# Performance work log

Hardware: AMD Instinct MI355X
Metric: run time of the kernel (lower is better)

The kernel has to match this reference:

```python
import jax, jax.numpy as jnp
import numpy as np

B, T, C = 8, 2048, 512

def setup_inputs() -> dict:
    key = jax.random.key(0)
    ks = jax.random.split(key, 16)
    def n(k, shape, s=0.02):
        return jax.random.normal(k, shape, dtype=jnp.float32) * s
    inp = {
        'x_l': jax.random.normal(ks[0], (B, T, C), jnp.float32),
        'x_r': jax.random.normal(ks[1], (B, T, C), jnp.float32),
    }
    i = 2
    for name in ['lp1', 'rp1', 'lp2', 'rp2']:
        inp[name + '_w1'] = n(ks[i], (C, C))       # pointwise conv1d weight (out,in)
        inp[name + '_b1'] = jnp.zeros((C,), jnp.float32)
        inp[name + '_w2'] = n(ks[i + 1], (C, 3))   # depthwise conv k=3 weight per channel
        inp[name + '_b2'] = jnp.zeros((C,), jnp.float32)
        i += 2
    inp['lp3_w'] = n(ks[i], (C, C)); inp['lp3_b'] = jnp.zeros((C,), jnp.float32)
    inp['rp3_w'] = n(ks[i + 1], (C, C)); inp['rp3_b'] = jnp.zeros((C,), jnp.float32)
    return inp

def _proj(x, w1, b1, w2, b2):
    # x: (B,T,C). Pointwise conv1d (1x1) then depthwise conv1d k=3, pad=1 over T.
    h = jnp.einsum('btc,dc->btd', x, w1) + b1
    hp = jnp.pad(h, ((0, 0), (1, 1), (0, 0)))
    # cross-correlation: tap 0 -> t-1, tap 1 -> t, tap 2 -> t+1 (matches torch Conv1d)
    return hp[:, :-2, :] * w2[:, 0] + hp[:, 1:-1, :] * w2[:, 1] + hp[:, 2:, :] * w2[:, 2] + b2

def reference(x_l, x_r,
              lp1_w1, lp1_b1, lp1_w2, lp1_b2,
              rp1_w1, rp1_b1, rp1_w2, rp1_b2,
              lp2_w1, lp2_b1, lp2_w2, lp2_b2,
              rp2_w1, rp2_b1, rp2_w2, rp2_b2,
              lp3_w, lp3_b, rp3_w, rp3_b):
    scale = C ** (-0.5)
    Q_l = _proj(x_l, lp1_w1, lp1_b1, lp1_w2, lp1_b2)  # (B,T,C)
    Q_r = _proj(x_r, rp1_w1, rp1_b1, rp1_w2, rp1_b2)  # (B,T,C)
    V_l = _proj(x_l, lp2_w1, lp2_b1, lp2_w2, lp2_b2)  # (B,T,C)
    V_r = _proj(x_r, rp2_w1, rp2_b1, rp2_w2, rp2_b2)  # (B,T,C)
    attn = jnp.einsum('btc,bsc->bts', Q_l, Q_r) * scale  # shared (B,T,T) scores
    # r->l: softmax over r-positions (last axis)
    F_r2l = jnp.einsum('bts,bsc->btc', jax.nn.softmax(attn, axis=-1), V_r)
    # l->r: softmax of attn^T over its last axis == softmax over axis 1 of attn
    F_l2r = jnp.einsum('bts,btc->bsc', jax.nn.softmax(attn, axis=1), V_l)
    out_l = x_l + jnp.einsum('btc,dc->btd', F_r2l, lp3_w) + lp3_b
    out_r = x_r + jnp.einsum('btc,dc->btd', F_l2r, rp3_w) + rp3_b
    return (out_l, out_r)
```

## Files before the change

kernel.cpp:

```cpp
#include <hip/hip_runtime.h>
#include <stdint.h>

#define Bb 8
#define Tt 2048
#define Cc 512

typedef __attribute__((ext_vector_type(8))) short short8;
typedef __attribute__((ext_vector_type(4))) short short4v;
typedef __attribute__((ext_vector_type(4))) float f32x4;

#define SZE ((size_t)Bb * Tt * Cc)

__device__ __forceinline__ float b2f(short s) {
  unsigned int x = ((unsigned int)(unsigned short)s) << 16;
  return __builtin_bit_cast(float, x);
}
__device__ __forceinline__ short f2b(float f) {
  unsigned int x = __builtin_bit_cast(unsigned int, f);
  x += 0x7fffu + ((x >> 16) & 1u);
  return (short)(x >> 16);
}

template<int MODE>
__global__ __launch_bounds__(256, 2)
void gemm_bt(const void* __restrict__ Av, const void* __restrict__ Av2,
             const void* __restrict__ Bv, const void* __restrict__ Bv2,
             void* __restrict__ Cv, void* __restrict__ Cv2,
             const float* __restrict__ bias,
             const float* __restrict__ resid, const float* __restrict__ resid2,
             short* __restrict__ ET, float* __restrict__ sumR, float* __restrict__ sumC,
             int M, int N, int K,
             long long sA, long long sB, long long sC, float scale)
{
  __shared__ __align__(16) short ldsA[8 * 128 * 8];
  __shared__ __align__(16) short ldsB[8 * 128 * 8];
  const int tid  = threadIdx.x;
  const int lane = tid & 63;

  int bxi = blockIdx.x, byi = blockIdx.y, bzi = blockIdx.z;
  const int gx = gridDim.x, gy = gridDim.y;
  if ((gy & 7) == 0) {
    int l = bxi + gx * (byi + gy * bzi);
    const int xcd = l & 7;
    int loc = l >> 3;
    const int ych = gy >> 3;
    bxi = loc % gx;  loc /= gx;
    byi = xcd * ych + (loc % ych);
    bzi = loc / ych;
  }

  const int bm = byi * 128;
  const int bn = bxi * 128;
  int dir = 0, zz = bzi;
  if constexpr (MODE == 2) { dir = bzi >> 3; zz = bzi & 7; }
  const long long zoA = (long long)zz * sA;
  const long long zoB = (long long)zz * sB;
  const long long zoC = (long long)zz * sC;
  const void* Ause = Av;
  const void* Buse = Bv;
  void* Cuse = Cv;
  const float* rp = resid;
  if constexpr (MODE == 0 || MODE == 3) {
    if (zz) { Ause = Av2; rp = resid2; }
  }
  if constexpr (MODE == 2) {
    if (dir) { Ause = Av2; Buse = Bv2; Cuse = Cv2; }
  }

  const int wv = tid >> 6;
  const int wm = (wv >> 1) << 6;
  const int wn = (wv & 1) << 6;

  f32x4 zero4 = {0.f, 0.f, 0.f, 0.f};
  f32x4 acc[4][4];
#pragma unroll
  for (int i = 0; i < 4; ++i)
#pragma unroll
    for (int j = 0; j < 4; ++j)
      acc[i][j] = zero4;

  const int sm  = tid >> 3;
  const int skc = tid & 7;

  for (int k0 = 0; k0 < K; k0 += 64) {
#pragma unroll
    for (int r = 0; r < 4; ++r) {
      const int m = r * 32 + sm;
      short8 av, bv;
      if constexpr (MODE == 0) {
        const float* ap = (const float*)Ause + zoA + (size_t)(bm + m) * K + k0 + skc * 8;
        float4 f0 = *(const float4*)ap;
        float4 f1 = *(const float4*)(ap + 4);
        av[0] = f2b(f0.x); av[1] = f2b(f0.y); av[2] = f2b(f0.z); av[3] = f2b(f0.w);
        av[4] = f2b(f1.x); av[5] = f2b(f1.y); av[6] = f2b(f1.z); av[7] = f2b(f1.w);
      } else {
        av = *(const short8*)((const short*)Ause + zoA + (size_t)(bm + m) * K + k0 + skc * 8);
      }
      bv = *(const short8*)((const short*)Buse + zoB + (size_t)(bn + m) * K + k0 + skc * 8);
      const int di = ((skc << 7) + (m ^ skc)) << 3;
      *(short8*)&ldsA[di] = av;
      *(short8*)&ldsB[di] = bv;
    }
    __syncthreads();
#pragma unroll
    for (int kk = 0; kk < 2; ++kk) {
      const int kcr = (kk << 2) + (lane >> 4);
      short8 af[4], bfv[4];
#pragma unroll
      for (int i = 0; i < 4; ++i) {
        const int ma = wm + i * 16 + (lane & 15);
        const int nb = wn + i * 16 + (lane & 15);
        af[i]  = *(const short8*)&ldsA[((kcr << 7) + (ma ^ kcr)) << 3];
        bfv[i] = *(const short8*)&ldsB[((kcr << 7) + (nb ^ kcr)) << 3];
      }
#pragma unroll
      for (int i = 0; i < 4; ++i)
#pragma unroll
        for (int j = 0; j < 4; ++j)
          acc[i][j] = __builtin_amdgcn_mfma_f32_16x16x32_bf16(af[i], bfv[j], acc[i][j], 0, 0, 0);
    }
    __syncthreads();
  }

  if constexpr (MODE == 4) {
#pragma unroll
    for (int i = 0; i < 4; ++i)
#pragma unroll
      for (int j = 0; j < 4; ++j)
#pragma unroll
        for (int r = 0; r < 4; ++r)
          acc[i][j][r] = __expf(acc[i][j][r] * scale);

#pragma unroll
    for (int i = 0; i < 4; ++i) {
      const int row0 = bm + wm + i * 16 + ((lane >> 4) << 2);
#pragma unroll
      for (int j = 0; j < 4; ++j) {
        const int n = bn + wn + j * 16 + (lane & 15);
        short4v t;
#pragma unroll
        for (int r = 0; r < 4; ++r) t[r] = f2b(acc[i][j][r]);
#pragma unroll
        for (int r = 0; r < 4; ++r)
          ((short*)Cv)[zoC + (size_t)(row0 + r) * N + n] = t[r];
        *(short4v*)(ET + zoC + (size_t)n * M + row0) = t;
      }
    }
#pragma unroll
    for (int i = 0; i < 4; ++i) {
      const int row0 = bm + wm + i * 16 + ((lane >> 4) << 2);
#pragma unroll
      for (int r = 0; r < 4; ++r) {
        float p = acc[i][0][r] + acc[i][1][r] + acc[i][2][r] + acc[i][3][r];
#pragma unroll
        for (int o = 1; o < 16; o <<= 1) p += __shfl_xor(p, o, 64);
        if ((lane & 15) == 0)
          unsafeAtomicAdd(&sumR[(size_t)zz * M + row0 + r], p);
      }
    }
#pragma unroll
    for (int j = 0; j < 4; ++j) {
      const int n = bn + wn + j * 16 + (lane & 15);
      float q = 0.f;
#pragma unroll
      for (int i = 0; i < 4; ++i)
#pragma unroll
        for (int r = 0; r < 4; ++r) q += acc[i][j][r];
      q += __shfl_xor(q, 16, 64);
      q += __shfl_xor(q, 32, 64);
      if (lane < 16)
        unsafeAtomicAdd(&sumC[(size_t)zz * N + n], q);
    }
  } else if constexpr (MODE == 2) {
    const float* sums = dir ? sumC : sumR;
#pragma unroll
    for (int i = 0; i < 4; ++i) {
      const int row0 = bm + wm + i * 16 + ((lane >> 4) << 2);
#pragma unroll
      for (int r = 0; r < 4; ++r) {
        const float iv = 1.0f / sums[(size_t)zz * M + row0 + r];
#pragma unroll
        for (int j = 0; j < 4; ++j) {
          const int n = bn + wn + j * 16 + (lane & 15);
          ((short*)Cuse)[zoC + (size_t)(row0 + r) * N + n] = f2b(acc[i][j][r] * iv);
        }
      }
    }
  } else {
#pragma unroll
    for (int i = 0; i < 4; ++i) {
      const int row0 = bm + wm + i * 16 + ((lane >> 4) << 2);
#pragma unroll
      for (int j = 0; j < 4; ++j) {
        const int n = bn + wn + j * 16 + (lane & 15);
        const float badd = bias[(size_t)zz * N + n];
#pragma unroll
        for (int r = 0; r < 4; ++r) {
          float val = acc[i][j][r] + badd;
          const size_t off = (size_t)(row0 + r) * N + n;
          if constexpr (MODE == 3) {
            ((float*)Cv)[zoC + off] = val + rp[off];
          } else {
            ((short*)Cv)[zoC + off] = f2b(val);
          }
        }
      }
    }
  }
  (void)scale; (void)ET; (void)sumR; (void)sumC; (void)Cuse; (void)rp;
}

__global__ __launch_bounds__(256)
void pack_all(const float* __restrict__ lw1a, const float* __restrict__ lw1b,
              const float* __restrict__ rw1a, const float* __restrict__ rw1b,
              const float* __restrict__ w3lf, const float* __restrict__ w3rf,
              const float* __restrict__ lb1a, const float* __restrict__ lb1b,
              const float* __restrict__ rb1a, const float* __restrict__ rb1b,
              const float* __restrict__ b3l, const float* __restrict__ b3r,
              short* __restrict__ Wl, short* __restrict__ Wr,
              short* __restrict__ W3l, short* __restrict__ W3r,
              float* __restrict__ BL, float* __restrict__ BR,
              float* __restrict__ B3, float* __restrict__ SUM)
{
  const int i = blockIdx.x * 256 + threadIdx.x;
  if (i < 524288) {
    Wl[i] = f2b(i < 262144 ? lw1a[i] : lw1b[i - 262144]);
  } else if (i < 1048576) {
    const int j = i - 524288;
    Wr[j] = f2b(j < 262144 ? rw1a[j] : rw1b[j - 262144]);
  } else if (i < 1310720) {
    W3l[i - 1048576] = f2b(w3lf[i - 1048576]);
  } else if (i < 1572864) {
    W3r[i - 1310720] = f2b(w3rf[i - 1310720]);
  } else if (i < 1573888) {
    const int j = i - 1572864;
    BL[j] = j < 512 ? lb1a[j] : lb1b[j - 512];
  } else if (i < 1574912) {
    const int j = i - 1573888;
    BR[j] = j < 512 ? rb1a[j] : rb1b[j - 512];
  } else if (i < 1575936) {
    const int j = i - 1574912;
    B3[j] = j < 512 ? b3l[j] : b3r[j - 512];
  } else if (i < 1608704) {
    SUM[i - 1575936] = 0.f;
  }
}

__global__ __launch_bounds__(256)
void dw_kernel(const short* __restrict__ H, long long hStride,
               const float* __restrict__ w2a, const float* __restrict__ w2b,
               const float* __restrict__ b2a, const float* __restrict__ b2b,
               short* __restrict__ out, int colOff)
{
  const int dir = blockIdx.y;
  const short* Hd = H + (size_t)dir * hStride;
  const float* w2 = dir ? w2b : w2a;
  const float* b2 = dir ? b2b : b2a;
  short* outd = out + (size_t)dir * SZE;

  const int idx = blockIdx.x * 256 + threadIdx.x;
  const int c8 = idx & 63;
  const int bt = idx >> 6;
  const int t  = bt & (Tt - 1);
  const int c  = c8 << 3;
  const short* base = Hd + (size_t)bt * 1024 + colOff + c;
  short8 zz = {0, 0, 0, 0, 0, 0, 0, 0};
  short8 hm = zz, hp = zz;
  short8 h0 = *(const short8*)base;
  if (t > 0)      hm = *(const short8*)(base - 1024);
  if (t < Tt - 1) hp = *(const short8*)(base + 1024);
  short8 o;
#pragma unroll
  for (int j = 0; j < 8; ++j) {
    const int cj = c + j;
    float val = b2f(hm[j]) * w2[cj * 3 + 0]
              + b2f(h0[j]) * w2[cj * 3 + 1]
              + b2f(hp[j]) * w2[cj * 3 + 2]
              + b2[cj];
    o[j] = f2b(val);
  }
  *(short8*)(outd + (size_t)bt * Cc + c) = o;
}

__global__ __launch_bounds__(256)
void dwt_kernel(const short* __restrict__ H, long long hStride,
                const float* __restrict__ w2a, const float* __restrict__ w2b,
                const float* __restrict__ b2a, const float* __restrict__ b2b,
                short* __restrict__ outT, int colOff)
{
  const int dir = blockIdx.z >> 3;
  const int b   = blockIdx.z & 7;
  const short* Hd = H + (size_t)dir * hStride;
  const float* w2 = dir ? w2b : w2a;
  const float* b2 = dir ? b2b : b2a;
  short* outd = outT + (size_t)dir * SZE;

  const int c  = blockIdx.y * 64 + (threadIdx.x & 63);
  const int tb = blockIdx.x * 32 + (threadIdx.x >> 6) * 8;
  const short* base = Hd + ((size_t)b * Tt) * 1024 + colOff + c;
  float h[10];
#pragma unroll
  for (int i = 0; i < 10; ++i) {
    const int t = tb - 1 + i;
    h[i] = (t >= 0 && t < Tt) ? b2f(base[(size_t)t * 1024]) : 0.f;
  }
  const float w0 = w2[c * 3 + 0];
  const float w1 = w2[c * 3 + 1];
  const float wp = w2[c * 3 + 2];
  const float bb = b2[c];
  short8 o;
#pragma unroll
  for (int j = 0; j < 8; ++j)
    o[j] = f2b(h[j] * w0 + h[j + 1] * w1 + h[j + 2] * wp + bb);
  *(short8*)(outd + ((size_t)b * Cc + c) * Tt + tb) = o;
}

extern "C" void kernel_launch(void* const* d_in, const int* in_sizes, int n_in,
                              void* d_out, int out_size, void* d_ws, size_t ws_size,
                              hipStream_t stream)
{
  const float* x_l    = (const float*)d_in[0];
  const float* x_r    = (const float*)d_in[1];
  const float* lp1_w1 = (const float*)d_in[2];
  const float* lp1_w2 = (const float*)d_in[4];
  const float* lp1_b2 = (const float*)d_in[5];
  const float* rp1_w1 = (const float*)d_in[6];
  const float* rp1_w2 = (const float*)d_in[8];
  const float* rp1_b2 = (const float*)d_in[9];
  const float* lp2_w1 = (const float*)d_in[10];
  const float* lp2_w2 = (const float*)d_in[12];
  const float* lp2_b2 = (const float*)d_in[13];
  const float* rp2_w1 = (const float*)d_in[14];
  const float* rp2_w2 = (const float*)d_in[16];
  const float* rp2_b2 = (const float*)d_in[17];
  const float* lp1_b1 = (const float*)d_in[3];
  const float* rp1_b1 = (const float*)d_in[7];
  const float* lp2_b1 = (const float*)d_in[11];
  const float* rp2_b1 = (const float*)d_in[15];
  const float* lp3_w  = (const float*)d_in[18];
  const float* lp3_b  = (const float*)d_in[19];
  const float* rp3_w  = (const float*)d_in[20];
  const float* rp3_b  = (const float*)d_in[21];

  short* ws = (short*)d_ws;
  const size_t SZ = SZE;
  short* Ql  = ws;
  short* Qr  = ws + SZ;
  short* VTl = ws + 2 * SZ;
  short* VTr = ws + 3 * SZ;
  short* E   = ws + 4 * SZ;
  short* ETb = ws + 8 * SZ;
  short* H   = E;
  short* Fb0 = Qr;
  short* Fb1 = Ql;

  const size_t W_PAIR = 524288, W_SING = 262144;
  short* Wl  = ws + 12 * SZ;
  short* Wr  = Wl + W_PAIR;
  short* W3l = Wr + W_PAIR;
  short* W3r = W3l + W_SING;
  float* BL  = (float*)(W3r + W_SING);
  float* BR  = BL + 1024;
  float* B3  = BR + 1024;
  float* SUMR = B3 + 1024;
  float* SUMC = SUMR + 16384;

  const float scale = 0.04419417382415922f;
  const int MT = Bb * Tt;
  const long long sQ = (long long)Tt * Cc;
  const long long sS = (long long)Tt * Tt;

  dim3 blk(256);

  pack_all<<<6284, blk, 0, stream>>>(lp1_w1, lp2_w1, rp1_w1, rp2_w1, lp3_w, rp3_w,
                                     lp1_b1, lp2_b1, rp1_b1, rp2_b1, lp3_b, rp3_b,
                                     Wl, Wr, W3l, W3r, BL, BR, B3, SUMR);

  gemm_bt<0><<<dim3(8, 128, 2), blk, 0, stream>>>(
      x_l, x_r, Wl, nullptr, H, nullptr, BL, nullptr, nullptr,
      nullptr, nullptr, nullptr,
      MT, 1024, Cc, 0, (long long)W_PAIR, (long long)(2 * SZ), 1.f);
  dw_kernel <<<dim3(4096, 2), blk, 0, stream>>>(
      H, (long long)(2 * SZ), lp1_w2, rp1_w2, lp1_b2, rp1_b2, Ql, 0);
  dwt_kernel<<<dim3(Tt / 32, 8, 2 * Bb), blk, 0, stream>>>(
      H, (long long)(2 * SZ), lp2_w2, rp2_w2, lp2_b2, rp2_b2, VTl, 512);

  gemm_bt<4><<<dim3(Tt / 128, Tt / 128, Bb), blk, 0, stream>>>(
      Ql, nullptr, Qr, nullptr, E, nullptr, nullptr, nullptr, nullptr,
      ETb, SUMR, SUMC,
      Tt, Tt, Cc, sQ, sQ, sS, scale);

  gemm_bt<2><<<dim3(Cc / 128, Tt / 128, 2 * Bb), blk, 0, stream>>>(
      E, ETb, VTr, VTl, Fb0, Fb1, nullptr, nullptr, nullptr,
      nullptr, SUMR, SUMC,
      Tt, Cc, Tt, sS, sQ, sQ, 1.f);

  gemm_bt<3><<<dim3(Cc / 128, MT / 128, 2), blk, 0, stream>>>(
      Fb0, Fb1, W3l, nullptr, d_out, nullptr, B3, x_l, x_r,
      nullptr, nullptr, nullptr,
      MT, Cc, Cc, 0, (long long)W_SING, (long long)SZ, 1.f);

  (void)in_sizes; (void)n_in; (void)out_size; (void)ws_size;
}
```

Measured before the change: 439.8 us.

## Reassociate output projection onto V before attention-weighted GEMM, fusing residual epilogue

The output projection is moved ahead of attention by reassociation: W3·(P·V) becomes P·(V·W3^T). A new GEMM computes the projected V in transposed layout, which removes both the transposed depthwise kernel and the final projection GEMM. The P·V GEMM now writes fp32 output directly, with bias and residual added in its epilogue. The four depthwise convolutions are merged into one launch. The new V-projection GEMM (M=512, N=2048 per batch) replaces the final GEMM (M=16384, N=512) at about the same FLOP count. Doing the projection before the softmax-weighted sum changes where bf16 rounding happens.

```diff
diff --git a/kernel.cpp b/kernel.cpp
--- a/kernel.cpp
+++ b/kernel.cpp
@@ -52,18 +52,17 @@
   const int bm = byi * 128;
   const int bn = bxi * 128;
   int dir = 0, zz = bzi;
-  if constexpr (MODE == 2) { dir = bzi >> 3; zz = bzi & 7; }
+  if constexpr (MODE == 1 || MODE == 2) { dir = bzi >> 3; zz = bzi & 7; }
   const long long zoA = (long long)zz * sA;
   const long long zoB = (long long)zz * sB;
   const long long zoC = (long long)zz * sC;
   const void* Ause = Av;
   const void* Buse = Bv;
   void* Cuse = Cv;
-  const float* rp = resid;
-  if constexpr (MODE == 0 || MODE == 3) {
-    if (zz) { Ause = Av2; rp = resid2; }
-  }
-  if constexpr (MODE == 2) {
+  if constexpr (MODE == 0) {
+    if (zz) Ause = Av2;
+  }
+  if constexpr (MODE == 1 || MODE == 2) {
     if (dir) { Ause = Av2; Buse = Bv2; Cuse = Cv2; }
   }
 
@@ -173,6 +172,7 @@
     }
   } else if constexpr (MODE == 2) {
     const float* sums = dir ? sumC : sumR;
+    const float* xr   = dir ? resid2 : resid;
 #pragma unroll
     for (int i = 0; i < 4; ++i) {
       const int row0 = bm + wm + i * 16 + ((lane >> 4) << 2);
@@ -182,7 +182,8 @@
 #pragma unroll
         for (int j = 0; j < 4; ++j) {
           const int n = bn + wn + j * 16 + (lane & 15);
-          ((short*)Cuse)[zoC + (size_t)(row0 + r) * N + n] = f2b(acc[i][j][r] * iv);
+          const size_t off = zoC + (size_t)(row0 + r) * N + n;
+          ((float*)Cuse)[off] = acc[i][j][r] * iv + bias[dir * N + n] + xr[off];
         }
       }
     }
@@ -193,21 +194,20 @@
 #pragma unroll
       for (int j = 0; j < 4; ++j) {
         const int n = bn + wn + j * 16 + (lane & 15);
-        const float badd = bias[(size_t)zz * N + n];
+        float badd = 0.f;
+        if (MODE == 0) badd = bias[(size_t)zz * N + n];
 #pragma unroll
         for (int r = 0; r < 4; ++r) {
-          float val = acc[i][j][r] + badd;
-          const size_t off = (size_t)(row0 + r) * N + n;
-          if constexpr (MODE == 3) {
-            ((float*)Cv)[zoC + off] = val + rp[off];
-          } else {
-            ((short*)Cv)[zoC + off] = f2b(val);
-          }
+          float val = acc[i][j][r];
+          if (MODE == 1) val *= scale;
+          if (MODE == 0) val += badd;
+          ((short*)Cuse)[zoC + (size_t)(row0 + r) * N + n] = f2b(val);
         }
       }
     }
   }
-  (void)scale; (void)ET; (void)sumR; (void)sumC; (void)Cuse; (void)rp;
+  (void)resid; (void)resid2; (void)ET; (void)sumR; (void)sumC;
+  (void)bias; (void)scale; (void)Cuse;
 }
 
 __global__ __launch_bounds__(256)
@@ -249,14 +249,17 @@
 __global__ __launch_bounds__(256)
 void dw_kernel(const short* __restrict__ H, long long hStride,
                const float* __restrict__ w2a, const float* __restrict__ w2b,
+               const float* __restrict__ w2c, const float* __restrict__ w2d,
                const float* __restrict__ b2a, const float* __restrict__ b2b,
-               short* __restrict__ out, int colOff)
+               const float* __restrict__ b2c, const float* __restrict__ b2d,
+               short* __restrict__ out)
 {
-  const int dir = blockIdx.y;
-  const short* Hd = H + (size_t)dir * hStride;
-  const float* w2 = dir ? w2b : w2a;
-  const float* b2 = dir ? b2b : b2a;
-  short* outd = out + (size_t)dir * SZE;
+  const int y = blockIdx.y;
+  const short* Hd = H + (size_t)(y & 1) * hStride;
+  const float* w2 = (y == 0) ? w2a : (y == 1) ? w2b : (y == 2) ? w2c : w2d;
+  const float* b2 = (y == 0) ? b2a : (y == 1) ? b2b : (y == 2) ? b2c : b2d;
+  const int colOff = (y & 2) ? 512 : 0;
+  short* outd = out + (size_t)y * SZE;
 
   const int idx = blockIdx.x * 256 + threadIdx.x;
   const int c8 = idx & 63;
@@ -264,8 +267,8 @@
   const int t  = bt & (Tt - 1);
   const int c  = c8 << 3;
   const short* base = Hd + (size_t)bt * 1024 + colOff + c;
-  short8 zz = {0, 0, 0, 0, 0, 0, 0, 0};
-  short8 hm = zz, hp = zz;
+  short8 zv = {0, 0, 0, 0, 0, 0, 0, 0};
+  short8 hm = zv, hp = zv;
   short8 h0 = *(const short8*)base;
   if (t > 0)      hm = *(const short8*)(base - 1024);
   if (t < Tt - 1) hp = *(const short8*)(base + 1024);
@@ -282,39 +285,6 @@
   *(short8*)(outd + (size_t)bt * Cc + c) = o;
 }
 
-__global__ __launch_bounds__(256)
-void dwt_kernel(const short* __restrict__ H, long long hStride,
-                const float* __restrict__ w2a, const float* __restrict__ w2b,
-                const float* __restrict__ b2a, const float* __restrict__ b2b,
-                short* __restrict__ outT, int colOff)
-{
-  const int dir = blockIdx.z >> 3;
-  const int b   = blockIdx.z & 7;
-  const short* Hd = H + (size_t)dir * hStride;
-  const float* w2 = dir ? w2b : w2a;
-  const float* b2 = dir ? b2b : b2a;
-  short* outd = outT + (size_t)dir * SZE;
-
-  const int c  = blockIdx.y * 64 + (threadIdx.x & 63);
-  const int tb = blockIdx.x * 32 + (threadIdx.x >> 6) * 8;
-  const short* base = Hd + ((size_t)b * Tt) * 1024 + colOff + c;
-  float h[10];
-#pragma unroll
-  for (int i = 0; i < 10; ++i) {
-    const int t = tb - 1 + i;
-    h[i] = (t >= 0 && t < Tt) ? b2f(base[(size_t)t * 1024]) : 0.f;
-  }
-  const float w0 = w2[c * 3 + 0];
-  const float w1 = w2[c * 3 + 1];
-  const float wp = w2[c * 3 + 2];
-  const float bb = b2[c];
-  short8 o;
-#pragma unroll
-  for (int j = 0; j < 8; ++j)
-    o[j] = f2b(h[j] * w0 + h[j + 1] * w1 + h[j + 2] * wp + bb);
-  *(short8*)(outd + ((size_t)b * Cc + c) * Tt + tb) = o;
-}
-
 extern "C" void kernel_launch(void* const* d_in, const int* in_sizes, int n_in,
                               void* d_out, int out_size, void* d_ws, size_t ws_size,
                               hipStream_t stream)
@@ -322,21 +292,21 @@
   const float* x_l    = (const float*)d_in[0];
   const float* x_r    = (const float*)d_in[1];
   const float* lp1_w1 = (const float*)d_in[2];
+  const float* lp1_b1 = (const float*)d_in[3];
   const float* lp1_w2 = (const float*)d_in[4];
   const float* lp1_b2 = (const float*)d_in[5];
   const float* rp1_w1 = (const float*)d_in[6];
+  const float* rp1_b1 = (const float*)d_in[7];
   const float* rp1_w2 = (const float*)d_in[8];
   const float* rp1_b2 = (const float*)d_in[9];
   const float* lp2_w1 = (const float*)d_in[10];
+  const float* lp2_b1 = (const float*)d_in[11];
   const float* lp2_w2 = (const float*)d_in[12];
   const float* lp2_b2 = (const float*)d_in[13];
   const float* rp2_w1 = (const float*)d_in[14];
+  const float* rp2_b1 = (const float*)d_in[15];
   const float* rp2_w2 = (const float*)d_in[16];
   const float* rp2_b2 = (const float*)d_in[17];
-  const float* lp1_b1 = (const float*)d_in[3];
-  const float* rp1_b1 = (const float*)d_in[7];
-  const float* lp2_b1 = (const float*)d_in[11];
-  const float* rp2_b1 = (const float*)d_in[15];
   const float* lp3_w  = (const float*)d_in[18];
   const float* lp3_b  = (const float*)d_in[19];
   const float* rp3_w  = (const float*)d_in[20];
@@ -344,15 +314,15 @@
 
   short* ws = (short*)d_ws;
   const size_t SZ = SZE;
-  short* Ql  = ws;
-  short* Qr  = ws + SZ;
-  short* VTl = ws + 2 * SZ;
-  short* VTr = ws + 3 * SZ;
-  short* E   = ws + 4 * SZ;
-  short* ETb = ws + 8 * SZ;
-  short* H   = E;
-  short* Fb0 = Qr;
-  short* Fb1 = Ql;
+  short* Ql   = ws;
+  short* Qr   = ws + SZ;
+  short* Vl   = ws + 2 * SZ;
+  short* Vr   = ws + 3 * SZ;
+  short* E    = ws + 4 * SZ;
+  short* ETb  = ws + 8 * SZ;
+  short* H    = E;
+  short* VWT0 = Ql;
+  short* VWT1 = Qr;
 
   const size_t W_PAIR = 524288, W_SING = 262144;
   short* Wl  = ws + 12 * SZ;
@@ -380,25 +350,25 @@
       x_l, x_r, Wl, nullptr, H, nullptr, BL, nullptr, nullptr,
       nullptr, nullptr, nullptr,
       MT, 1024, Cc, 0, (long long)W_PAIR, (long long)(2 * SZ), 1.f);
-  dw_kernel <<<dim3(4096, 2), blk, 0, stream>>>(
-      H, (long long)(2 * SZ), lp1_w2, rp1_w2, lp1_b2, rp1_b2, Ql, 0);
-  dwt_kernel<<<dim3(Tt / 32, 8, 2 * Bb), blk, 0, stream>>>(
-      H, (long long)(2 * SZ), lp2_w2, rp2_w2, lp2_b2, rp2_b2, VTl, 512);
+  dw_kernel<<<dim3(4096, 4), blk, 0, stream>>>(
+      H, (long long)(2 * SZ),
+      lp1_w2, rp1_w2, lp2_w2, rp2_w2,
+      lp1_b2, rp1_b2, lp2_b2, rp2_b2, Ql);
 
   gemm_bt<4><<<dim3(Tt / 128, Tt / 128, Bb), blk, 0, stream>>>(
       Ql, nullptr, Qr, nullptr, E, nullptr, nullptr, nullptr, nullptr,
       ETb, SUMR, SUMC,
       Tt, Tt, Cc, sQ, sQ, sS, scale);
 
+  gemm_bt<1><<<dim3(Tt / 128, 4, 2 * Bb), blk, 0, stream>>>(
+      W3l, W3r, Vr, Vl, VWT0, VWT1, nullptr, nullptr, nullptr,
+      nullptr, nullptr, nullptr,
+      512, Tt, Cc, 0, sQ, (long long)(512 * Tt), 1.f);
+
   gemm_bt<2><<<dim3(Cc / 128, Tt / 128, 2 * Bb), blk, 0, stream>>>(
-      E, ETb, VTr, VTl, Fb0, Fb1, nullptr, nullptr, nullptr,
+      E, ETb, VWT0, VWT1, d_out, (float*)d_out + SZ, B3, x_l, x_r,
       nullptr, SUMR, SUMC,
-      Tt, Cc, Tt, sS, sQ, sQ, 1.f);
-
-  gemm_bt<3><<<dim3(Cc / 128, MT / 128, 2), blk, 0, stream>>>(
-      Fb0, Fb1, W3l, nullptr, d_out, nullptr, B3, x_l, x_r,
-      nullptr, nullptr, nullptr,
-      MT, Cc, Cc, 0, (long long)W_SING, (long long)SZ, 1.f);
+      Tt, Cc, Tt, sS, (long long)(512 * Tt), sQ, 1.f);
 
   (void)in_sizes; (void)n_in; (void)out_size; (void)ws_size;
 }
```

New measurement: 441.6 us. No clear change (+0.4%).
